# Kernel tuning notes

Hardware: AMD Instinct MI355X
Metric: run time of the kernel (lower is better)

## Reference

```python
import jax, jax.numpy as jnp
import numpy as np

F = 65536          # num_face
W_DIM = 512
PAD = 4096         # zero pad rows appended before gather
LRELU_SLOPE = 0.2
LRELU_GAIN = np.sqrt(2.0).astype(np.float32)  # def_gain of lrelu


def _fc(w, W, b):
    # StyleGAN FullyConnectedLayer: x @ W.T / sqrt(in_features) + bias
    gain = np.float32(1.0 / np.sqrt(W.shape[1]))
    return w @ W.T * gain + b


def _faceconv_gather(x, neigh, is_pad, k):
    # x: [B*F, C]; neigh/is_pad: [B*F, 9]; take first k neighbor slots.
    padded = jnp.concatenate([x, jnp.zeros((PAD, x.shape[1]), x.dtype)], axis=0)
    g = padded[neigh[:, :k]]                      # [B*F, k, C] irregular gather
    return jnp.where(is_pad[:, :k, None], jnp.zeros((), x.dtype), g)


def _modulated_face_conv(g, weight, styles, demodulate):
    # g: [B*F, k, I]; weight: [O, I, 1, k]; styles: [B, I]
    B = styles.shape[0]
    w = weight[None, :, :, 0, :] * styles[:, None, :, None]      # [B, O, I, k]
    if demodulate:
        d = jax.lax.rsqrt(jnp.sum(w * w, axis=(2, 3)) + 1e-8)    # [B, O]
        w = w * d[:, :, None, None]
    gb = g.reshape(B, -1, g.shape[1], g.shape[2])                # [B, F, k, I]
    out = jnp.einsum('bfki,boik->bfo', gb, w)                    # [B, F, O]
    return out.reshape(-1, w.shape[1])


def setup_inputs() -> dict:
    key = jax.random.key(0)
    ks = jax.random.split(key, 12)
    B = 2
    C = 128
    N = B * F
    face_neighborhood = jax.random.randint(ks[0], (N, 9), 0, N + PAD, dtype=jnp.int64)
    face_is_pad = jax.random.randint(ks[1], (N, 9), 0, 10) == 0
    return {
        'face_neighborhood': face_neighborhood,
        'face_is_pad': face_is_pad,
        'ws': jax.random.normal(ks[2], (B, 2, W_DIM), jnp.float32),
        'const': jax.random.normal(ks[3], (F, C), jnp.float32),
        'affine1_W': jax.random.normal(ks[4], (C, W_DIM), jnp.float32),
        'affine1_b': jnp.ones((C,), jnp.float32),
        'weight1': jax.random.normal(ks[5], (C, C, 1, 9), jnp.float32),
        'noise_const': jax.random.normal(ks[6], (F,), jnp.float32),
        'noise_strength': jnp.zeros((1,), jnp.float32),
        'bias1': jnp.zeros((C,), jnp.float32),
        'affine2_W': jax.random.normal(ks[7], (C, W_DIM), jnp.float32),
        'affine2_b': jnp.ones((C,), jnp.float32),
        'weight2': jax.random.normal(ks[8], (3, C, 1, 1), jnp.float32),
        'bias2': jnp.zeros((3,), jnp.float32),
    }


def reference(face_neighborhood, face_is_pad, ws, const, affine1_W, affine1_b,
              weight1, noise_const, noise_strength, bias1, affine2_W, affine2_b,
              weight2, bias2):
    # noise_mode == 'const'
    B = ws.shape[0]
    w0, w1 = ws[:, 0], ws[:, 1]
    x = jnp.tile(const[None], (B, 1, 1)).reshape(B * F, -1)        # [B*F, C]

    # --- SynthesisLayer conv1 ---
    styles = _fc(w0, affine1_W, affine1_b)                         # [B, C]
    noise = jnp.tile(noise_const[None], (B, 1)).reshape(-1, 1) * noise_strength
    g = _faceconv_gather(x, face_neighborhood, face_is_pad, 9)     # [B*F, 9, C]
    x = _modulated_face_conv(g, weight1, styles, demodulate=True)  # [B*F, C]
    x = x + noise
    x = jax.nn.leaky_relu(x + bias1[None, :], LRELU_SLOPE)
    x = jnp.clip(x * LRELU_GAIN, -256.0, 256.0)                    # clamp_gain

    # --- ToRGBLayer ---
    wg = np.float32(1.0 / np.sqrt(weight2.shape[1] * 1))
    styles2 = _fc(w1, affine2_W, affine2_b) * wg
    g2 = _faceconv_gather(x, face_neighborhood, face_is_pad, 1)    # [B*F, 1, C]
    img = _modulated_face_conv(g2, weight2, styles2, demodulate=False)
    img = jnp.clip(img + bias2[None, :], -256.0, 256.0)
    return x, img
```

## Files before the change

kernel.cpp:

```cpp
#include <hip/hip_runtime.h>

typedef unsigned short u16;
typedef __bf16 bf16x8 __attribute__((ext_vector_type(8)));
typedef float f32x4 __attribute__((ext_vector_type(4)));
typedef unsigned short u16x8 __attribute__((ext_vector_type(8)));

#define F_FACES 65536
#define N_FACES 131072
#define C_CH 128
#define WS_W2F 256
#define WS_S1 3328
#define WS_W1 4352
#define WS_CONST 594176
#define XELEMS 16777216

__device__ inline u16 f2bf(float f) {
    unsigned u = __builtin_bit_cast(unsigned, f);
    unsigned r = (u + 0x7fffu + ((u >> 16) & 1u)) >> 16;
    return (u16)r;
}

__device__ inline void gl_lds16(const void* g, void* l) {
    __builtin_amdgcn_global_load_lds(
        (const __attribute__((address_space(1))) void*)g,
        (__attribute__((address_space(3))) void*)l, 16, 0, 0);
}

__global__ __launch_bounds__(256) void k0_styles(
    const float* __restrict__ wsv, const float* __restrict__ a1W, const float* __restrict__ a1b,
    const float* __restrict__ a2W, const float* __restrict__ a2b, const float* __restrict__ w2,
    unsigned char* __restrict__ wsb)
{
    __shared__ float s2s[256];
    int t = threadIdx.x;
    int b = t >> 7, o = t & 127;
    const float* w0r = wsv + (b * 2 + 0) * 512;
    const float* w1r = wsv + (b * 2 + 1) * 512;
    const float* r1 = a1W + o * 512;
    const float* r2 = a2W + o * 512;
    float s1 = 0.f, s2 = 0.f;
    for (int j = 0; j < 512; j += 4) {
        float4 x0 = *(const float4*)(w0r + j);
        float4 x1 = *(const float4*)(w1r + j);
        float4 y1 = *(const float4*)(r1 + j);
        float4 y2 = *(const float4*)(r2 + j);
        s1 += x0.x * y1.x + x0.y * y1.y + x0.z * y1.z + x0.w * y1.w;
        s2 += x1.x * y2.x + x1.y * y2.y + x1.z * y2.z + x1.w * y2.w;
    }
    const float g512 = 0.04419417382415922f;
    const float g128 = 0.08838834764831845f;
    float st1 = s1 * g512 + a1b[o];
    float st2 = (s2 * g512 + a2b[o]) * g128;
    float* wsf = (float*)wsb;
    wsf[WS_S1 / 4 + t] = st1;
    s2s[t] = st2;
    if (t < 64) wsf[t] = 0.f;
    __syncthreads();
#pragma unroll
    for (int r = 0; r < 3; ++r) {
        int id = t + r * 256;
        int b2 = id / 384;
        int rem = id - b2 * 384;
        int o2 = rem >> 7;
        int i = rem & 127;
        wsf[WS_W2F / 4 + id] = w2[o2 * 128 + i] * s2s[b2 * 128 + i];
    }
}

__global__ __launch_bounds__(64) void k0b_fold(
    const float* __restrict__ w1g, const float* __restrict__ s1base, u16* __restrict__ w1out)
{
    int bo = blockIdx.x;
    int b = bo >> 7, o = bo & 127;
    int l = threadIdx.x;
    const float* s1 = s1base + b * 128;
    float sum = 0.f;
    for (int e = l; e < 1152; e += 64) {
        int i = e / 9;
        float w = w1g[o * 1152 + e] * s1[i];
        sum += w * w;
    }
#pragma unroll
    for (int d = 1; d < 64; d <<= 1) sum += __shfl_xor(sum, d);
    float dm = rsqrtf(sum + 1e-8f);
    int i0 = l * 2;
    float sa = s1[i0] * dm, sb = s1[i0 + 1] * dm;
#pragma unroll
    for (int k = 0; k < 9; ++k) {
        float v0 = w1g[(o * 128 + i0) * 9 + k] * sa;
        float v1 = w1g[(o * 128 + i0 + 1) * 9 + k] * sb;
        unsigned pack = (unsigned)f2bf(v0) | ((unsigned)f2bf(v1) << 16);
        *(unsigned*)&w1out[(size_t)(((b * 9 + k) * 128 + o) * 128) + i0] = pack;
    }
}

__global__ __launch_bounds__(256) void k_cvt(
    const float* __restrict__ src, u16* __restrict__ dst)
{
    int t = blockIdx.x * 256 + threadIdx.x;
    int base = t * 8;
    float4 a = *(const float4*)(src + base);
    float4 c = *(const float4*)(src + base + 4);
    u16x8 p;
    p[0] = f2bf(a.x); p[1] = f2bf(a.y); p[2] = f2bf(a.z); p[3] = f2bf(a.w);
    p[4] = f2bf(c.x); p[5] = f2bf(c.y); p[6] = f2bf(c.z); p[7] = f2bf(c.w);
    *(u16x8*)(dst + base) = p;
}

__global__ __launch_bounds__(256, 2) void k1_conv(
    const int* __restrict__ neigh, const int* __restrict__ ispad,
    const float* __restrict__ noise_c, const float* __restrict__ nstr,
    const float* __restrict__ bias1, const unsigned char* __restrict__ wsb,
    float* __restrict__ out)
{
    __shared__ u16 As[128 * 128];
    __shared__ u16 Bs[128 * 128];

    int tid = threadIdx.x;
    int wv = tid >> 6, lane = tid & 63;
    int quad = lane >> 4, l15 = lane & 15;
    int f0 = blockIdx.x * 128;
    int b = f0 >> 16;
    const u16* cst = (const u16*)(wsb + WS_CONST);
    const u16* w1ws = (const u16*)(wsb + WS_W1) + (size_t)b * 147456;
    const char* zp = (const char*)wsb;

    int nidx[8];
    int cg16[8];
    int brow[8];
    int ldso[8];
#pragma unroll
    for (int r = 0; r < 8; ++r) {
        int cid = ((wv * 8 + r) << 6) + lane;
        int row = cid >> 4;
        int slot = cid & 15;
        nidx[r] = (f0 + row) * 9;
        cg16[r] = ((slot ^ (row & 15)) << 4);
        brow[r] = row << 8;
        ldso[r] = (wv * 8 + r) << 10;
    }

    f32x4 acc[4][4] = {};
    int wm = wv & 1, wn = wv >> 1;

    for (int k = 0; k < 9; ++k) {
        __syncthreads();
#pragma unroll
        for (int r = 0; r < 8; ++r) {
            int idx = neigh[nidx[r] + k];
            bool valid = (ispad[nidx[r] + k] == 0) && ((unsigned)idx < 131072u);
            const char* src = valid ? ((const char*)(cst + ((size_t)(idx & 65535) << 7))) : zp;
            gl_lds16(src + cg16[r], (char*)As + ldso[r]);
        }
        const char* bsrc = (const char*)(w1ws + k * 16384);
#pragma unroll
        for (int r = 0; r < 8; ++r) {
            gl_lds16(bsrc + brow[r] + cg16[r], (char*)Bs + ldso[r]);
        }
        __syncthreads();
#pragma unroll
        for (int s = 0; s < 4; ++s) {
            bf16x8 af[4], bfr[4];
#pragma unroll
            for (int mt = 0; mt < 4; ++mt) {
                int face = wm * 64 + mt * 16 + l15;
                int chunk = (s * 4 + quad) ^ (face & 15);
                af[mt] = *reinterpret_cast<const bf16x8*>(&As[face * 128 + chunk * 8]);
            }
#pragma unroll
            for (int nt = 0; nt < 4; ++nt) {
                int o = wn * 64 + nt * 16 + l15;
                int chunk = (s * 4 + quad) ^ (o & 15);
                bfr[nt] = *reinterpret_cast<const bf16x8*>(&Bs[o * 128 + chunk * 8]);
            }
#pragma unroll
            for (int mt = 0; mt < 4; ++mt)
#pragma unroll
                for (int nt = 0; nt < 4; ++nt)
                    acc[mt][nt] = __builtin_amdgcn_mfma_f32_16x16x32_bf16(
                        af[mt], bfr[nt], acc[mt][nt], 0, 0, 0);
        }
    }

    float ns = nstr[0];
    float b1v[4];
#pragma unroll
    for (int nt = 0; nt < 4; ++nt) b1v[nt] = bias1[wn * 64 + nt * 16 + l15];
#pragma unroll
    for (int mt = 0; mt < 4; ++mt) {
#pragma unroll
        for (int r = 0; r < 4; ++r) {
            int face = f0 + wm * 64 + mt * 16 + quad * 4 + r;
            float nz = noise_c[face & 65535] * ns;
#pragma unroll
            for (int nt = 0; nt < 4; ++nt) {
                float v = acc[mt][nt][r] + nz + b1v[nt];
                v = (v > 0.f) ? v : 0.2f * v;
                v *= 1.41421356f;
                v = fminf(fmaxf(v, -256.f), 256.f);
                out[(size_t)face * 128 + wn * 64 + nt * 16 + l15] = v;
            }
        }
    }
}

__global__ __launch_bounds__(256) void k2_img(
    const int* __restrict__ neigh, const int* __restrict__ ispad,
    const float* __restrict__ w2f, const float* __restrict__ bias2,
    const float* __restrict__ xbuf, float* __restrict__ imgout)
{
    int tid = threadIdx.x;
    int wv = tid >> 6, lane = tid & 63;
    int g = lane >> 4, sub = lane & 15;
    int face = blockIdx.x * 16 + wv * 4 + g;
    int b = face >> 16;
    float w[3][8];
#pragma unroll
    for (int o = 0; o < 3; ++o)
#pragma unroll
        for (int j = 0; j < 8; ++j) w[o][j] = w2f[(b * 3 + o) * 128 + sub * 8 + j];
    int idx = neigh[face * 9];
    bool valid = (ispad[face * 9] == 0) && ((unsigned)idx < 131072u);
    float a0 = 0.f, a1 = 0.f, a2 = 0.f;
    if (valid) {
        float4 d0 = *(const float4*)(xbuf + (size_t)idx * 128 + sub * 8);
        float4 d1 = *(const float4*)(xbuf + (size_t)idx * 128 + sub * 8 + 4);
        float f[8] = {d0.x, d0.y, d0.z, d0.w, d1.x, d1.y, d1.z, d1.w};
#pragma unroll
        for (int j = 0; j < 8; ++j) {
            a0 += f[j] * w[0][j];
            a1 += f[j] * w[1][j];
            a2 += f[j] * w[2][j];
        }
    }
#pragma unroll
    for (int d = 1; d < 16; d <<= 1) {
        a0 += __shfl_xor(a0, d);
        a1 += __shfl_xor(a1, d);
        a2 += __shfl_xor(a2, d);
    }
    if (sub < 3) {
        float v = (sub == 0) ? a0 : (sub == 1) ? a1 : a2;
        v += bias2[sub];
        v = fminf(fmaxf(v, -256.f), 256.f);
        imgout[face * 3 + sub] = v;
    }
}

extern "C" void kernel_launch(void* const* d_in, const int* in_sizes, int n_in,
                              void* d_out, int out_size, void* d_ws, size_t ws_size,
                              hipStream_t stream) {
    const int* neigh = (const int*)d_in[0];
    const int* ispad = (const int*)d_in[1];
    const float* wsv = (const float*)d_in[2];
    const float* cst = (const float*)d_in[3];
    const float* a1W = (const float*)d_in[4];
    const float* a1b = (const float*)d_in[5];
    const float* w1g = (const float*)d_in[6];
    const float* noise_c = (const float*)d_in[7];
    const float* nstr = (const float*)d_in[8];
    const float* bias1 = (const float*)d_in[9];
    const float* a2W = (const float*)d_in[10];
    const float* a2b = (const float*)d_in[11];
    const float* w2 = (const float*)d_in[12];
    const float* bias2 = (const float*)d_in[13];
    float* out = (float*)d_out;
    unsigned char* wsb = (unsigned char*)d_ws;

    k0_styles<<<1, 256, 0, stream>>>(wsv, a1W, a1b, a2W, a2b, w2, wsb);
    k0b_fold<<<256, 64, 0, stream>>>(w1g, (const float*)(wsb + WS_S1), (u16*)(wsb + WS_W1));
    k_cvt<<<4096, 256, 0, stream>>>(cst, (u16*)(wsb + WS_CONST));
    k1_conv<<<1024, 256, 0, stream>>>(neigh, ispad, noise_c, nstr, bias1, wsb, out);
    k2_img<<<8192, 256, 0, stream>>>(neigh, ispad, (const float*)(wsb + WS_W2F), bias2,
                                     out, out + XELEMS);
}
```

Before: 237.1 us.

## Parallelize style FC, stream conv weights from global, cache ToRGB weights in LDS

```diff
diff --git a/kernel.cpp b/kernel.cpp
--- a/kernel.cpp
+++ b/kernel.cpp
@@ -10,8 +10,9 @@
 #define C_CH 128
 #define WS_W2F 256
 #define WS_S1 3328
-#define WS_W1 4352
-#define WS_CONST 594176
+#define WS_S2 4352
+#define WS_W1 5376
+#define WS_CONST 595200
 #define XELEMS 16777216
 
 __device__ inline u16 f2bf(float f) {
@@ -26,36 +27,41 @@
         (__attribute__((address_space(3))) void*)l, 16, 0, 0);
 }
 
-__global__ __launch_bounds__(256) void k0_styles(
+__global__ __launch_bounds__(256) void k0a_styles(
     const float* __restrict__ wsv, const float* __restrict__ a1W, const float* __restrict__ a1b,
-    const float* __restrict__ a2W, const float* __restrict__ a2b, const float* __restrict__ w2,
-    unsigned char* __restrict__ wsb)
-{
-    __shared__ float s2s[256];
+    const float* __restrict__ a2W, const float* __restrict__ a2b, unsigned char* __restrict__ wsb)
+{
+    int wv = threadIdx.x >> 6, lane = threadIdx.x & 63;
+    int c = blockIdx.x * 4 + wv;
+    int which = c >> 8, rem = c & 255, b = rem >> 7, o = rem & 127;
+    const float* W = (which ? a2W : a1W) + o * 512 + lane * 8;
+    const float* x = wsv + (b * 2 + which) * 512 + lane * 8;
+    float4 wa = *(const float4*)(W);
+    float4 wb = *(const float4*)(W + 4);
+    float4 xa = *(const float4*)(x);
+    float4 xb = *(const float4*)(x + 4);
+    float s = wa.x * xa.x + wa.y * xa.y + wa.z * xa.z + wa.w * xa.w
+            + wb.x * xb.x + wb.y * xb.y + wb.z * xb.z + wb.w * xb.w;
+#pragma unroll
+    for (int d = 1; d < 64; d <<= 1) s += __shfl_xor(s, d);
+    if (lane == 0) {
+        const float g512 = 0.04419417382415922f;
+        const float g128 = 0.08838834764831845f;
+        float* wsf = (float*)wsb;
+        if (which == 0) {
+            wsf[WS_S1 / 4 + b * 128 + o] = s * g512 + a1b[o];
+        } else {
+            wsf[WS_S2 / 4 + b * 128 + o] = (s * g512 + a2b[o]) * g128;
+        }
+    }
+}
+
+__global__ __launch_bounds__(256) void k0w_fold2(
+    const float* __restrict__ w2, unsigned char* __restrict__ wsb)
+{
     int t = threadIdx.x;
-    int b = t >> 7, o = t & 127;
-    const float* w0r = wsv + (b * 2 + 0) * 512;
-    const float* w1r = wsv + (b * 2 + 1) * 512;
-    const float* r1 = a1W + o * 512;
-    const float* r2 = a2W + o * 512;
-    float s1 = 0.f, s2 = 0.f;
-    for (int j = 0; j < 512; j += 4) {
-        float4 x0 = *(const float4*)(w0r + j);
-        float4 x1 = *(const float4*)(w1r + j);
-        float4 y1 = *(const float4*)(r1 + j);
-        float4 y2 = *(const float4*)(r2 + j);
-        s1 += x0.x * y1.x + x0.y * y1.y + x0.z * y1.z + x0.w * y1.w;
-        s2 += x1.x * y2.x + x1.y * y2.y + x1.z * y2.z + x1.w * y2.w;
-    }
-    const float g512 = 0.04419417382415922f;
-    const float g128 = 0.08838834764831845f;
-    float st1 = s1 * g512 + a1b[o];
-    float st2 = (s2 * g512 + a2b[o]) * g128;
     float* wsf = (float*)wsb;
-    wsf[WS_S1 / 4 + t] = st1;
-    s2s[t] = st2;
     if (t < 64) wsf[t] = 0.f;
-    __syncthreads();
 #pragma unroll
     for (int r = 0; r < 3; ++r) {
         int id = t + r * 256;
@@ -63,17 +69,17 @@
         int rem = id - b2 * 384;
         int o2 = rem >> 7;
         int i = rem & 127;
-        wsf[WS_W2F / 4 + id] = w2[o2 * 128 + i] * s2s[b2 * 128 + i];
+        wsf[WS_W2F / 4 + id] = w2[o2 * 128 + i] * wsf[WS_S2 / 4 + b2 * 128 + i];
     }
 }
 
 __global__ __launch_bounds__(64) void k0b_fold(
-    const float* __restrict__ w1g, const float* __restrict__ s1base, u16* __restrict__ w1out)
+    const float* __restrict__ w1g, const unsigned char* __restrict__ wsb, u16* __restrict__ w1out)
 {
     int bo = blockIdx.x;
     int b = bo >> 7, o = bo & 127;
     int l = threadIdx.x;
-    const float* s1 = s1base + b * 128;
+    const float* s1 = (const float*)(wsb + WS_S1) + b * 128;
     float sum = 0.f;
     for (int e = l; e < 1152; e += 64) {
         int i = e / 9;
@@ -85,12 +91,13 @@
     float dm = rsqrtf(sum + 1e-8f);
     int i0 = l * 2;
     float sa = s1[i0] * dm, sb = s1[i0 + 1] * dm;
+    int chunk = i0 >> 3, j = i0 & 7;
 #pragma unroll
     for (int k = 0; k < 9; ++k) {
         float v0 = w1g[(o * 128 + i0) * 9 + k] * sa;
         float v1 = w1g[(o * 128 + i0 + 1) * 9 + k] * sb;
         unsigned pack = (unsigned)f2bf(v0) | ((unsigned)f2bf(v1) << 16);
-        *(unsigned*)&w1out[(size_t)(((b * 9 + k) * 128 + o) * 128) + i0] = pack;
+        *(unsigned*)&w1out[(size_t)((((b * 9 + k) * 16 + chunk) * 128 + o) * 8 + j)] = pack;
     }
 }
 
@@ -107,14 +114,13 @@
     *(u16x8*)(dst + base) = p;
 }
 
-__global__ __launch_bounds__(256, 2) void k1_conv(
+__global__ __launch_bounds__(256, 4) void k1_conv(
     const int* __restrict__ neigh, const int* __restrict__ ispad,
     const float* __restrict__ noise_c, const float* __restrict__ nstr,
     const float* __restrict__ bias1, const unsigned char* __restrict__ wsb,
     float* __restrict__ out)
 {
     __shared__ u16 As[128 * 128];
-    __shared__ u16 Bs[128 * 128];
 
     int tid = threadIdx.x;
     int wv = tid >> 6, lane = tid & 63;
@@ -125,21 +131,6 @@
     const u16* w1ws = (const u16*)(wsb + WS_W1) + (size_t)b * 147456;
     const char* zp = (const char*)wsb;
 
-    int nidx[8];
-    int cg16[8];
-    int brow[8];
-    int ldso[8];
-#pragma unroll
-    for (int r = 0; r < 8; ++r) {
-        int cid = ((wv * 8 + r) << 6) + lane;
-        int row = cid >> 4;
-        int slot = cid & 15;
-        nidx[r] = (f0 + row) * 9;
-        cg16[r] = ((slot ^ (row & 15)) << 4);
-        brow[r] = row << 8;
-        ldso[r] = (wv * 8 + r) << 10;
-    }
-
     f32x4 acc[4][4] = {};
     int wm = wv & 1, wn = wv >> 1;
 
@@ -147,15 +138,14 @@
         __syncthreads();
 #pragma unroll
         for (int r = 0; r < 8; ++r) {
-            int idx = neigh[nidx[r] + k];
-            bool valid = (ispad[nidx[r] + k] == 0) && ((unsigned)idx < 131072u);
+            int cid = ((wv * 8 + r) << 6) + lane;
+            int row = cid >> 4;
+            int slot = cid & 15;
+            int nb = (f0 + row) * 9 + k;
+            int idx = neigh[nb];
+            bool valid = (ispad[nb] == 0) && ((unsigned)idx < 131072u);
             const char* src = valid ? ((const char*)(cst + ((size_t)(idx & 65535) << 7))) : zp;
-            gl_lds16(src + cg16[r], (char*)As + ldso[r]);
-        }
-        const char* bsrc = (const char*)(w1ws + k * 16384);
-#pragma unroll
-        for (int r = 0; r < 8; ++r) {
-            gl_lds16(bsrc + brow[r] + cg16[r], (char*)Bs + ldso[r]);
+            gl_lds16(src + ((slot ^ (row & 15)) << 4), (char*)As + ((wv * 8 + r) << 10));
         }
         __syncthreads();
 #pragma unroll
@@ -167,12 +157,10 @@
                 int chunk = (s * 4 + quad) ^ (face & 15);
                 af[mt] = *reinterpret_cast<const bf16x8*>(&As[face * 128 + chunk * 8]);
             }
-#pragma unroll
-            for (int nt = 0; nt < 4; ++nt) {
-                int o = wn * 64 + nt * 16 + l15;
-                int chunk = (s * 4 + quad) ^ (o & 15);
-                bfr[nt] = *reinterpret_cast<const bf16x8*>(&Bs[o * 128 + chunk * 8]);
-            }
+            const u16* bp = w1ws + (((k * 16 + s * 4 + quad) * 128) + wn * 64 + l15) * 8;
+#pragma unroll
+            for (int nt = 0; nt < 4; ++nt)
+                bfr[nt] = *reinterpret_cast<const bf16x8*>(bp + nt * 128);
 #pragma unroll
             for (int mt = 0; mt < 4; ++mt)
 #pragma unroll
@@ -209,16 +197,16 @@
     const float* __restrict__ w2f, const float* __restrict__ bias2,
     const float* __restrict__ xbuf, float* __restrict__ imgout)
 {
+    __shared__ float ws2[768];
     int tid = threadIdx.x;
+    ws2[tid] = w2f[tid];
+    ws2[tid + 256] = w2f[tid + 256];
+    ws2[tid + 512] = w2f[tid + 512];
+    __syncthreads();
     int wv = tid >> 6, lane = tid & 63;
     int g = lane >> 4, sub = lane & 15;
     int face = blockIdx.x * 16 + wv * 4 + g;
     int b = face >> 16;
-    float w[3][8];
-#pragma unroll
-    for (int o = 0; o < 3; ++o)
-#pragma unroll
-        for (int j = 0; j < 8; ++j) w[o][j] = w2f[(b * 3 + o) * 128 + sub * 8 + j];
     int idx = neigh[face * 9];
     bool valid = (ispad[face * 9] == 0) && ((unsigned)idx < 131072u);
     float a0 = 0.f, a1 = 0.f, a2 = 0.f;
@@ -226,11 +214,14 @@
         float4 d0 = *(const float4*)(xbuf + (size_t)idx * 128 + sub * 8);
         float4 d1 = *(const float4*)(xbuf + (size_t)idx * 128 + sub * 8 + 4);
         float f[8] = {d0.x, d0.y, d0.z, d0.w, d1.x, d1.y, d1.z, d1.w};
+        const float* w0 = &ws2[(b * 3 + 0) * 128 + sub * 8];
+        const float* w1 = &ws2[(b * 3 + 1) * 128 + sub * 8];
+        const float* w2p = &ws2[(b * 3 + 2) * 128 + sub * 8];
 #pragma unroll
         for (int j = 0; j < 8; ++j) {
-            a0 += f[j] * w[0][j];
-            a1 += f[j] * w[1][j];
-            a2 += f[j] * w[2][j];
+            a0 += f[j] * w0[j];
+            a1 += f[j] * w1[j];
+            a2 += f[j] * w2p[j];
         }
     }
 #pragma unroll
@@ -267,8 +258,9 @@
     float* out = (float*)d_out;
     unsigned char* wsb = (unsigned char*)d_ws;
 
-    k0_styles<<<1, 256, 0, stream>>>(wsv, a1W, a1b, a2W, a2b, w2, wsb);
-    k0b_fold<<<256, 64, 0, stream>>>(w1g, (const float*)(wsb + WS_S1), (u16*)(wsb + WS_W1));
+    k0a_styles<<<128, 256, 0, stream>>>(wsv, a1W, a1b, a2W, a2b, wsb);
+    k0w_fold2<<<1, 256, 0, stream>>>(w2, wsb);
+    k0b_fold<<<256, 64, 0, stream>>>(w1g, wsb, (u16*)(wsb + WS_W1));
     k_cvt<<<4096, 256, 0, stream>>>(cst, (u16*)(wsb + WS_CONST));
     k1_conv<<<1024, 256, 0, stream>>>(neigh, ispad, noise_c, nstr, bias1, wsb, out);
     k2_img<<<8192, 256, 0, stream>>>(neigh, ispad, (const float*)(wsb + WS_W2F), bias2,
```

Measured after the change: 234.2 us. No clear change (-1.2%).
